# Kernel optimization log

Measured on AMD Instinct MI355X. Metric: run time of the kernel, lower is better.

## Reference

```python
import jax, jax.numpy as jnp
import numpy as np

B, N = 64, 4096

def setup_inputs() -> dict:
    key = jax.random.key(0)
    k1, k2, k3, k4, k5, k6 = jax.random.split(key, 6)
    return {
        "V_mag": jax.random.uniform(k1, (B, N), dtype=jnp.float32, minval=0.9, maxval=1.1),
        "V_ang": 0.3 * jax.random.normal(k2, (B, N), dtype=jnp.float32),
        "P_in": jax.random.normal(k3, (B, N), dtype=jnp.float32),
        "Q_in": jax.random.normal(k4, (B, N), dtype=jnp.float32),
        "G_bus": jax.random.normal(k5, (N, N), dtype=jnp.float32) / np.sqrt(N),
        "B_bus": jax.random.normal(k6, (N, N), dtype=jnp.float32) / np.sqrt(N),
    }

def reference(V_mag, V_ang, P_in, Q_in, G_bus, B_bus):
    # P_i = V_i sum_j V_j (G_ij cos(ti-tj) + B_ij sin(ti-tj))
    # Q_i = V_i sum_j V_j (G_ij sin(ti-tj) - B_ij cos(ti-tj))
    # Angle-addition rewrite (exact): with c_j = V_j cos(t_j), s_j = V_j sin(t_j):
    #   sum_j G_ij V_j cos(ti-tj) = cos(ti)*(G c)_i + sin(ti)*(G s)_i, etc.
    cos_t = jnp.cos(V_ang)  # [B, N]
    sin_t = jnp.sin(V_ang)
    c = V_mag * cos_t       # V_j cos(t_j)
    s = V_mag * sin_t       # V_j sin(t_j)
    Gc = jnp.einsum('ij,bj->bi', G_bus, c)
    Gs = jnp.einsum('ij,bj->bi', G_bus, s)
    Bc = jnp.einsum('ij,bj->bi', B_bus, c)
    Bs = jnp.einsum('ij,bj->bi', B_bus, s)
    # sum_j V_j (G cos + B sin) = cos_ti*(Gc+Bs) + sin_ti*(Gs-Bc)
    P_calc = V_mag * (cos_t * (Gc + Bs) + sin_t * (Gs - Bc))
    # sum_j V_j (G sin - B cos) = sin_ti*(Gc+Bs) - cos_ti*(Gs-Bc)
    Q_calc = V_mag * (sin_t * (Gc + Bs) - cos_t * (Gs - Bc))
    res_P = P_calc - P_in
    res_Q = Q_calc - Q_in
    return (res_P, res_Q)
```

## Files before the change

kernel.cpp:

```cpp
#include <hip/hip_runtime.h>
#include <stdint.h>

#define N_DIM 4096
#define B_DIM 64

typedef __bf16 bf16x8 __attribute__((ext_vector_type(8)));
typedef float floatx4 __attribute__((ext_vector_type(4)));

union FragU { uint4 u; bf16x8 h; };

#define AS1 __attribute__((address_space(1)))
#define AS3 __attribute__((address_space(3)))

__device__ __forceinline__ void gll16(const float* gp, float* lp) {
    __builtin_amdgcn_global_load_lds((const AS1 void*)(const void*)gp,
                                     (AS3 void*)(void*)lp, 16, 0, 0);
}

__device__ __forceinline__ unsigned short f2bf_rne(float f) {
    unsigned int u = __float_as_uint(f);
    u += 0x7fffu + ((u >> 16) & 1u);
    return (unsigned short)(u >> 16);
}

__global__ __launch_bounds__(256) void pf_prep(
        const float* __restrict__ Vmag, const float* __restrict__ Vang,
        unsigned short* __restrict__ c_pk, unsigned short* __restrict__ s_pk,
        float* __restrict__ c_f, float* __restrict__ s_f) {
    int idx = blockIdx.x * 256 + threadIdx.x;
    int b = idx >> 12;
    int j = idx & 4095;
    float sv, cv;
    sincosf(Vang[idx], &sv, &cv);
    float v = Vmag[idx];
    float c = v * cv;
    float s = v * sv;
    c_f[idx] = c;
    s_f[idx] = s;
    int p = (((j >> 3) << 6) + b) * 8 + (j & 7);
    c_pk[p] = f2bf_rne(c);
    s_pk[p] = f2bf_rne(s);
}

#define ROWF 516
#define MATF (16 * ROWF)
#define BUFF (2 * MATF)
__global__ __launch_bounds__(1024, 4) void pf_gemm(
        const float* __restrict__ G, const float* __restrict__ Bm,
        const unsigned short* __restrict__ c_pk, const unsigned short* __restrict__ s_pk,
        const float* __restrict__ c_f, const float* __restrict__ s_f,
        const float* __restrict__ P_in, const float* __restrict__ Q_in,
        float* __restrict__ out) {
    __shared__ __align__(16) float lds_f[2 * BUFF];
    const int tid = threadIdx.x;
    const int wave = tid >> 6;
    const int lane = tid & 63;
    const int n = lane & 15;
    const int quad = lane >> 4;
    const int i0 = blockIdx.x << 4;

    const float* gsrc = G  + (size_t)(i0 + wave) * N_DIM + lane * 4;
    const float* bsrc = Bm + (size_t)(i0 + wave) * N_DIM + lane * 4;
    const int stg = wave * ROWF;

    const int aoff = n * ROWF + wave * 32 + quad * 8;

    const unsigned short* cp = c_pk + ((size_t)(((wave << 2) + quad) << 6) + n) * 8;
    const unsigned short* sp = s_pk + ((size_t)(((wave << 2) + quad) << 6) + n) * 8;

    floatx4 accX[4], accY[4];
    #pragma unroll
    for (int t = 0; t < 4; ++t) {
        accX[t] = (floatx4){0.f, 0.f, 0.f, 0.f};
        accY[t] = (floatx4){0.f, 0.f, 0.f, 0.f};
    }

    gll16(gsrc,       lds_f + stg);
    gll16(gsrc + 256, lds_f + stg + 256);
    gll16(bsrc,       lds_f + MATF + stg);
    gll16(bsrc + 256, lds_f + MATF + stg + 256);

    #pragma unroll 2
    for (int c = 0; c < 8; ++c) {
        const int buf = (c & 1) * BUFF;
        __syncthreads();

        if (c < 7) {
            const int nb = ((c + 1) & 1) * BUFF;
            const float* gs = gsrc + (c + 1) * 512;
            const float* bs = bsrc + (c + 1) * 512;
            gll16(gs,       lds_f + nb + stg);
            gll16(gs + 256, lds_f + nb + stg + 256);
            gll16(bs,       lds_f + nb + MATF + stg);
            gll16(bs + 256, lds_f + nb + MATF + stg + 256);
        }

        const float* ga = lds_f + buf + aoff;
        const float* ba = lds_f + buf + MATF + aoff;
        float4 g0 = *(const float4*)ga;
        float4 g1 = *(const float4*)(ga + 4);
        float4 h0 = *(const float4*)ba;
        float4 h1 = *(const float4*)(ba + 4);
        bf16x8 ag, ah;
        ag[0] = (__bf16)g0.x; ag[1] = (__bf16)g0.y; ag[2] = (__bf16)g0.z; ag[3] = (__bf16)g0.w;
        ag[4] = (__bf16)g1.x; ag[5] = (__bf16)g1.y; ag[6] = (__bf16)g1.z; ag[7] = (__bf16)g1.w;
        ah[0] = (__bf16)h0.x; ah[1] = (__bf16)h0.y; ah[2] = (__bf16)h0.z; ah[3] = (__bf16)h0.w;
        ah[4] = (__bf16)h1.x; ah[5] = (__bf16)h1.y; ah[6] = (__bf16)h1.z; ah[7] = (__bf16)h1.w;

        uint4 cu[4];
        #pragma unroll
        for (int t = 0; t < 4; ++t) cu[t] = *(const uint4*)(cp + (size_t)c * 32768 + t * 128);
        #pragma unroll
        for (int t = 0; t < 4; ++t) {
            FragU cf, nf;
            cf.u = cu[t];
            nf.u.x = cu[t].x ^ 0x80008000u;
            nf.u.y = cu[t].y ^ 0x80008000u;
            nf.u.z = cu[t].z ^ 0x80008000u;
            nf.u.w = cu[t].w ^ 0x80008000u;
            accX[t] = __builtin_amdgcn_mfma_f32_16x16x32_bf16(ag, cf.h, accX[t], 0, 0, 0);
            accY[t] = __builtin_amdgcn_mfma_f32_16x16x32_bf16(ah, nf.h, accY[t], 0, 0, 0);
        }

        uint4 su[4];
        #pragma unroll
        for (int t = 0; t < 4; ++t) su[t] = *(const uint4*)(sp + (size_t)c * 32768 + t * 128);
        #pragma unroll
        for (int t = 0; t < 4; ++t) {
            FragU sf;
            sf.u = su[t];
            accX[t] = __builtin_amdgcn_mfma_f32_16x16x32_bf16(ah, sf.h, accX[t], 0, 0, 0);
            accY[t] = __builtin_amdgcn_mfma_f32_16x16x32_bf16(ag, sf.h, accY[t], 0, 0, 0);
        }
    }

    float* red = lds_f;
    #define RED(x, wp, m, b) red[(((x) * 8 + (wp)) * 16 + (m)) * 66 + (b)]
    __syncthreads();
    if (wave >= 8) {
        #pragma unroll
        for (int t = 0; t < 4; ++t)
            #pragma unroll
            for (int r = 0; r < 4; ++r) {
                RED(0, wave - 8, (quad << 2) + r, (t << 4) + n) = accX[t][r];
                RED(1, wave - 8, (quad << 2) + r, (t << 4) + n) = accY[t][r];
            }
    }
    __syncthreads();
    if (wave < 8) {
        #pragma unroll
        for (int t = 0; t < 4; ++t)
            #pragma unroll
            for (int r = 0; r < 4; ++r) {
                RED(0, wave, (quad << 2) + r, (t << 4) + n) += accX[t][r];
                RED(1, wave, (quad << 2) + r, (t << 4) + n) += accY[t][r];
            }
    }
    __syncthreads();

    {
        int bb = tid >> 4;
        int m = tid & 15;
        float X = 0.f, Y = 0.f;
        #pragma unroll
        for (int w = 0; w < 8; ++w) {
            X += RED(0, w, m, bb);
            Y += RED(1, w, m, bb);
        }
        size_t off = (size_t)bb * N_DIM + i0 + m;
        float c = c_f[off], s = s_f[off];
        out[off] = c * X + s * Y - P_in[off];
        out[(size_t)B_DIM * N_DIM + off] = s * X - c * Y - Q_in[off];
    }
}

extern "C" void kernel_launch(void* const* d_in, const int* in_sizes, int n_in,
                              void* d_out, int out_size, void* d_ws, size_t ws_size,
                              hipStream_t stream) {
    const float* Vmag = (const float*)d_in[0];
    const float* Vang = (const float*)d_in[1];
    const float* P_in = (const float*)d_in[2];
    const float* Q_in = (const float*)d_in[3];
    const float* G    = (const float*)d_in[4];
    const float* Bm   = (const float*)d_in[5];
    float* out = (float*)d_out;

    char* ws = (char*)d_ws;
    unsigned short* c_pk = (unsigned short*)(ws);
    unsigned short* s_pk = (unsigned short*)(ws + (512u << 10));
    float* c_f = (float*)(ws + (1u << 20));
    float* s_f = (float*)(ws + (2u << 20));

    hipLaunchKernelGGL(pf_prep, dim3((B_DIM * N_DIM) / 256), dim3(256), 0, stream,
                       Vmag, Vang, c_pk, s_pk, c_f, s_f);
    hipLaunchKernelGGL(pf_gemm, dim3(N_DIM / 16), dim3(1024), 0, stream,
                       G, Bm, c_pk, s_pk, c_f, s_f, P_in, Q_in, out);
}
```

Measured before the change: 165.7 us.

## Load G/B fragments straight from global, dropping the LDS staging pipeline and fp32 c/s buffers

The GEMM kernel stops staging G and B rows through double-buffered LDS with global_load_lds and per-chunk barriers. Each lane now loads its A fragment directly from global memory, with a register prefetch of the next K-step, and each wave covers a contiguous K range. The prep kernel no longer writes fp32 c/s arrays; the epilogue recomputes sincos from Vmag/Vang instead. This removes LDS traffic and syncs, but the direct global loads are strided across rows, so coalescing may be worse.

```diff
diff --git a/kernel.cpp b/kernel.cpp
--- a/kernel.cpp
+++ b/kernel.cpp
@@ -9,14 +9,6 @@
 
 union FragU { uint4 u; bf16x8 h; };
 
-#define AS1 __attribute__((address_space(1)))
-#define AS3 __attribute__((address_space(3)))
-
-__device__ __forceinline__ void gll16(const float* gp, float* lp) {
-    __builtin_amdgcn_global_load_lds((const AS1 void*)(const void*)gp,
-                                     (AS3 void*)(void*)lp, 16, 0, 0);
-}
-
 __device__ __forceinline__ unsigned short f2bf_rne(float f) {
     unsigned int u = __float_as_uint(f);
     u += 0x7fffu + ((u >> 16) & 1u);
@@ -25,33 +17,25 @@
 
 __global__ __launch_bounds__(256) void pf_prep(
         const float* __restrict__ Vmag, const float* __restrict__ Vang,
-        unsigned short* __restrict__ c_pk, unsigned short* __restrict__ s_pk,
-        float* __restrict__ c_f, float* __restrict__ s_f) {
+        unsigned short* __restrict__ c_pk, unsigned short* __restrict__ s_pk) {
     int idx = blockIdx.x * 256 + threadIdx.x;
     int b = idx >> 12;
     int j = idx & 4095;
     float sv, cv;
     sincosf(Vang[idx], &sv, &cv);
     float v = Vmag[idx];
-    float c = v * cv;
-    float s = v * sv;
-    c_f[idx] = c;
-    s_f[idx] = s;
     int p = (((j >> 3) << 6) + b) * 8 + (j & 7);
-    c_pk[p] = f2bf_rne(c);
-    s_pk[p] = f2bf_rne(s);
+    c_pk[p] = f2bf_rne(v * cv);
+    s_pk[p] = f2bf_rne(v * sv);
 }
 
-#define ROWF 516
-#define MATF (16 * ROWF)
-#define BUFF (2 * MATF)
-__global__ __launch_bounds__(1024, 4) void pf_gemm(
+__global__ __launch_bounds__(1024) void pf_gemm(
         const float* __restrict__ G, const float* __restrict__ Bm,
         const unsigned short* __restrict__ c_pk, const unsigned short* __restrict__ s_pk,
-        const float* __restrict__ c_f, const float* __restrict__ s_f,
+        const float* __restrict__ Vmag, const float* __restrict__ Vang,
         const float* __restrict__ P_in, const float* __restrict__ Q_in,
         float* __restrict__ out) {
-    __shared__ __align__(16) float lds_f[2 * BUFF];
+    __shared__ __align__(16) float red[2 * 8 * 16 * 66];
     const int tid = threadIdx.x;
     const int wave = tid >> 6;
     const int lane = tid & 63;
@@ -59,14 +43,10 @@
     const int quad = lane >> 4;
     const int i0 = blockIdx.x << 4;
 
-    const float* gsrc = G  + (size_t)(i0 + wave) * N_DIM + lane * 4;
-    const float* bsrc = Bm + (size_t)(i0 + wave) * N_DIM + lane * 4;
-    const int stg = wave * ROWF;
-
-    const int aoff = n * ROWF + wave * 32 + quad * 8;
-
-    const unsigned short* cp = c_pk + ((size_t)(((wave << 2) + quad) << 6) + n) * 8;
-    const unsigned short* sp = s_pk + ((size_t)(((wave << 2) + quad) << 6) + n) * 8;
+    const float* gp = G  + (size_t)(i0 + n) * N_DIM + wave * 256 + quad * 8;
+    const float* bp = Bm + (size_t)(i0 + n) * N_DIM + wave * 256 + quad * 8;
+    const unsigned short* cp = c_pk + ((size_t)(wave * 32 + quad) * 64 + n) * 8;
+    const unsigned short* sp = s_pk + ((size_t)(wave * 32 + quad) * 64 + n) * 8;
 
     floatx4 accX[4], accY[4];
     #pragma unroll
@@ -75,68 +55,62 @@
         accY[t] = (floatx4){0.f, 0.f, 0.f, 0.f};
     }
 
-    gll16(gsrc,       lds_f + stg);
-    gll16(gsrc + 256, lds_f + stg + 256);
-    gll16(bsrc,       lds_f + MATF + stg);
-    gll16(bsrc + 256, lds_f + MATF + stg + 256);
+    float4 g0 = *(const float4*)(gp);
+    float4 g1 = *(const float4*)(gp + 4);
+    float4 h0 = *(const float4*)(bp);
+    float4 h1 = *(const float4*)(bp + 4);
 
-    #pragma unroll 2
-    for (int c = 0; c < 8; ++c) {
-        const int buf = (c & 1) * BUFF;
-        __syncthreads();
-
-        if (c < 7) {
-            const int nb = ((c + 1) & 1) * BUFF;
-            const float* gs = gsrc + (c + 1) * 512;
-            const float* bs = bsrc + (c + 1) * 512;
-            gll16(gs,       lds_f + nb + stg);
-            gll16(gs + 256, lds_f + nb + stg + 256);
-            gll16(bs,       lds_f + nb + MATF + stg);
-            gll16(bs + 256, lds_f + nb + MATF + stg + 256);
+    #pragma unroll
+    for (int t = 0; t < 8; ++t) {
+        float4 ng0, ng1, nh0, nh1;
+        if (t < 7) {
+            const float* g2 = gp + (t + 1) * 32;
+            const float* b2 = bp + (t + 1) * 32;
+            ng0 = *(const float4*)(g2);
+            ng1 = *(const float4*)(g2 + 4);
+            nh0 = *(const float4*)(b2);
+            nh1 = *(const float4*)(b2 + 4);
         }
 
-        const float* ga = lds_f + buf + aoff;
-        const float* ba = lds_f + buf + MATF + aoff;
-        float4 g0 = *(const float4*)ga;
-        float4 g1 = *(const float4*)(ga + 4);
-        float4 h0 = *(const float4*)ba;
-        float4 h1 = *(const float4*)(ba + 4);
         bf16x8 ag, ah;
         ag[0] = (__bf16)g0.x; ag[1] = (__bf16)g0.y; ag[2] = (__bf16)g0.z; ag[3] = (__bf16)g0.w;
         ag[4] = (__bf16)g1.x; ag[5] = (__bf16)g1.y; ag[6] = (__bf16)g1.z; ag[7] = (__bf16)g1.w;
         ah[0] = (__bf16)h0.x; ah[1] = (__bf16)h0.y; ah[2] = (__bf16)h0.z; ah[3] = (__bf16)h0.w;
         ah[4] = (__bf16)h1.x; ah[5] = (__bf16)h1.y; ah[6] = (__bf16)h1.z; ah[7] = (__bf16)h1.w;
 
+        const unsigned short* cpt = cp + (size_t)t * 2048;
+        const unsigned short* spt = sp + (size_t)t * 2048;
+
         uint4 cu[4];
         #pragma unroll
-        for (int t = 0; t < 4; ++t) cu[t] = *(const uint4*)(cp + (size_t)c * 32768 + t * 128);
+        for (int t16 = 0; t16 < 4; ++t16) cu[t16] = *(const uint4*)(cpt + t16 * 128);
         #pragma unroll
-        for (int t = 0; t < 4; ++t) {
+        for (int t16 = 0; t16 < 4; ++t16) {
             FragU cf, nf;
-            cf.u = cu[t];
-            nf.u.x = cu[t].x ^ 0x80008000u;
-            nf.u.y = cu[t].y ^ 0x80008000u;
-            nf.u.z = cu[t].z ^ 0x80008000u;
-            nf.u.w = cu[t].w ^ 0x80008000u;
-            accX[t] = __builtin_amdgcn_mfma_f32_16x16x32_bf16(ag, cf.h, accX[t], 0, 0, 0);
-            accY[t] = __builtin_amdgcn_mfma_f32_16x16x32_bf16(ah, nf.h, accY[t], 0, 0, 0);
+            cf.u = cu[t16];
+            nf.u.x = cu[t16].x ^ 0x80008000u;
+            nf.u.y = cu[t16].y ^ 0x80008000u;
+            nf.u.z = cu[t16].z ^ 0x80008000u;
+            nf.u.w = cu[t16].w ^ 0x80008000u;
+            accX[t16] = __builtin_amdgcn_mfma_f32_16x16x32_bf16(ag, cf.h, accX[t16], 0, 0, 0);
+            accY[t16] = __builtin_amdgcn_mfma_f32_16x16x32_bf16(ah, nf.h, accY[t16], 0, 0, 0);
         }
 
         uint4 su[4];
         #pragma unroll
-        for (int t = 0; t < 4; ++t) su[t] = *(const uint4*)(sp + (size_t)c * 32768 + t * 128);
+        for (int t16 = 0; t16 < 4; ++t16) su[t16] = *(const uint4*)(spt + t16 * 128);
         #pragma unroll
-        for (int t = 0; t < 4; ++t) {
+        for (int t16 = 0; t16 < 4; ++t16) {
             FragU sf;
-            sf.u = su[t];
-            accX[t] = __builtin_amdgcn_mfma_f32_16x16x32_bf16(ah, sf.h, accX[t], 0, 0, 0);
-            accY[t] = __builtin_amdgcn_mfma_f32_16x16x32_bf16(ag, sf.h, accY[t], 0, 0, 0);
+            sf.u = su[t16];
+            accX[t16] = __builtin_amdgcn_mfma_f32_16x16x32_bf16(ah, sf.h, accX[t16], 0, 0, 0);
+            accY[t16] = __builtin_amdgcn_mfma_f32_16x16x32_bf16(ag, sf.h, accY[t16], 0, 0, 0);
         }
+
+        g0 = ng0; g1 = ng1; h0 = nh0; h1 = nh1;
     }
 
-    float* red = lds_f;
     #define RED(x, wp, m, b) red[(((x) * 8 + (wp)) * 16 + (m)) * 66 + (b)]
-    __syncthreads();
     if (wave >= 8) {
         #pragma unroll
         for (int t = 0; t < 4; ++t)
@@ -168,7 +142,11 @@
             Y += RED(1, w, m, bb);
         }
         size_t off = (size_t)bb * N_DIM + i0 + m;
-        float c = c_f[off], s = s_f[off];
+        float sv, cv;
+        sincosf(Vang[off], &sv, &cv);
+        float v = Vmag[off];
+        float c = v * cv;
+        float s = v * sv;
         out[off] = c * X + s * Y - P_in[off];
         out[(size_t)B_DIM * N_DIM + off] = s * X - c * Y - Q_in[off];
     }
@@ -188,11 +166,9 @@
     char* ws = (char*)d_ws;
     unsigned short* c_pk = (unsigned short*)(ws);
     unsigned short* s_pk = (unsigned short*)(ws + (512u << 10));
-    float* c_f = (float*)(ws + (1u << 20));
-    float* s_f = (float*)(ws + (2u << 20));
 
     hipLaunchKernelGGL(pf_prep, dim3((B_DIM * N_DIM) / 256), dim3(256), 0, stream,
-                       Vmag, Vang, c_pk, s_pk, c_f, s_f);
+                       Vmag, Vang, c_pk, s_pk);
     hipLaunchKernelGGL(pf_gemm, dim3(N_DIM / 16), dim3(1024), 0, stream,
-                       G, Bm, c_pk, s_pk, c_f, s_f, P_in, Q_in, out);
+                       G, Bm, c_pk, s_pk, Vmag, Vang, P_in, Q_in, out);
 }
```

After: 174.3 us. 1.05x slower.
